# Kernel tuning notes

Hardware: AMD Instinct MI355X
Metric: run time of the kernel (lower is better)

Reference implementation:

```python
import jax, jax.numpy as jnp
import numpy as np
from jax import lax

relu = jax.nn.relu

def _conv2d(x, w, b, stride=1, pad=1):
    y = lax.conv_general_dilated(x, w, (stride, stride), [(pad, pad), (pad, pad)],
                                 dimension_numbers=('NCHW', 'OIHW', 'NCHW'))
    return y + b[None, :, None, None]

def _convT2d(x, wt, b):
    # PyTorch ConvTranspose2d(k=4, stride=2, padding=1) == dilated conv with flipped, transposed weight
    w = jnp.flip(wt, (2, 3)).transpose(1, 0, 2, 3)  # (out,in,4,4)
    y = lax.conv_general_dilated(x, w, (1, 1), [(2, 2), (2, 2)], lhs_dilation=(2, 2),
                                 dimension_numbers=('NCHW', 'OIHW', 'NCHW'))
    return y + b[None, :, None, None]

def _conv3d(x, w, b):
    y = lax.conv_general_dilated(x, w, (1, 1, 1), [(1, 1), (1, 1), (1, 1)],
                                 dimension_numbers=('NCDHW', 'OIDHW', 'NCDHW'))
    return y + b[None, :, None, None, None]

def _bilinear(x, py, px):
    # x: (B,C,H,W); py/px: (B,C,K,H,W) fractional sample coords; zero padding outside
    B, C, H, W = x.shape
    y0 = jnp.floor(py)
    x0 = jnp.floor(px)
    y0i = y0.astype(jnp.int32)
    x0i = x0.astype(jnp.int32)
    wy1 = py - y0
    wx1 = px - x0
    wy0 = 1.0 - wy1
    wx0 = 1.0 - wx1

    def corner(yi, xi):
        valid = (yi >= 0) & (yi < H) & (xi >= 0) & (xi < W)
        yc = jnp.clip(yi, 0, H - 1)
        xc = jnp.clip(xi, 0, W - 1)
        gather = lambda img, yy, xx: img[yy, xx]  # (H,W),(K,H,W)->(K,H,W)
        v = jax.vmap(jax.vmap(gather))(x, yc, xc)
        return jnp.where(valid, v, 0.0)

    return (wy0 * wx0 * corner(y0i, x0i) + wy0 * wx1 * corner(y0i, x0i + 1)
            + wy1 * wx0 * corner(y0i + 1, x0i) + wy1 * wx1 * corner(y0i + 1, x0i + 1))

def _deform_conv(x, off, msk, w, b, ks=3):
    # Modulated deformable conv v2, stride 1, pad ks//2, deformable_groups = C (1 channel/group)
    B, C, H, W = x.shape
    K = ks * ks
    pad = ks // 2
    off = off.reshape(B, C, K, 2, H, W)  # per group/kernel-point (dy, dx)
    dy = off[:, :, :, 0]
    dx = off[:, :, :, 1]
    ki, kj = jnp.meshgrid(jnp.arange(ks), jnp.arange(ks), indexing='ij')
    ky = (ki.reshape(-1) - pad).astype(x.dtype)  # (K,)
    kx = (kj.reshape(-1) - pad).astype(x.dtype)
    gy = jnp.arange(H, dtype=x.dtype)
    gx = jnp.arange(W, dtype=x.dtype)
    py = gy[None, None, None, :, None] + ky[None, None, :, None, None] + dy
    px = gx[None, None, None, None, :] + kx[None, None, :, None, None] + dx
    sampled = _bilinear(x, py, px) * msk.reshape(B, C, K, H, W)  # (B,C,K,H,W)
    out = jnp.einsum('bckhw,ock->bohw', sampled, w.reshape(w.shape[0], C, K))
    return out + b[None, :, None, None]

def _forward(inputs, w_in, b_in, w_dn1a, b_dn1a, w_dn1b, b_dn1b, w_dn2a, b_dn2a, w_dn2b, b_dn2b,
             w_up1a, b_up1a, wt_up1, bt_up1, w_up2a, b_up2a, wt_up2, bt_up2,
             w_tra, b_tra, w_trb, b_trb, wt_tr, bt_tr, w_out, b_out,
             w_tf3a, b_tf3a, w_tf3b, b_tf3b, w_tf2, b_tf2, w_om, b_om, w_dc, b_dc):
    C = inputs.shape[1]
    K = 9
    # U-shape encoder
    f0 = relu(_conv2d(inputs, w_in, b_in))
    f1 = relu(_conv2d(relu(_conv2d(f0, w_dn1a, b_dn1a, stride=2)), w_dn1b, b_dn1b))
    f2 = relu(_conv2d(relu(_conv2d(f1, w_dn2a, b_dn2a, stride=2)), w_dn2b, b_dn2b))
    # trunk
    t = relu(_conv2d(f2, w_tra, b_tra, stride=2))
    t = relu(_conv2d(t, w_trb, b_trb))
    t = relu(_convT2d(t, wt_tr, bt_tr))
    # decoder with skip concats
    t = relu(_conv2d(jnp.concatenate([t, f2], axis=1), w_up2a, b_up2a))
    t = relu(_convT2d(t, wt_up2, bt_up2))
    t = relu(_conv2d(jnp.concatenate([t, f1], axis=1), w_up1a, b_up1a))
    t = relu(_convT2d(t, wt_up1, bt_up1))
    # temporal fusion (Conv3d over frames, mean-pool depth)
    x3 = inputs[:, None]  # (B,1,D,H,W)
    x3 = relu(_conv3d(x3, w_tf3a, b_tf3a))
    x3 = relu(_conv3d(x3, w_tf3b, b_tf3b))
    tf = _conv2d(x3.mean(axis=2), w_tf2, b_tf2)
    fused = relu(t + tf)
    om = _conv2d(relu(_conv2d(fused, w_out, b_out)), w_om, b_om)
    off = om[:, :C * 2 * K]
    msk = jax.nn.sigmoid(om[:, C * 2 * K:])
    return relu(_deform_conv(inputs, off, msk, w_dc, b_dc, 3))

def setup_inputs() -> dict:
    key = jax.random.key(0)
    cnt = [0]
    def rn(shape, scale=0.05):
        cnt[0] += 1
        return scale * jax.random.normal(jax.random.fold_in(key, cnt[0]), shape, dtype=jnp.float32)
    B, C, H, W, nf, out_nc = 2, 7, 160, 160, 32, 64
    z = lambda n: jnp.zeros((n,), jnp.float32)
    d = {'inputs': rn((B, C, H, W), 1.0)}
    d['w_in'] = rn((nf, C, 3, 3)); d['b_in'] = z(nf)
    for i in (1, 2):
        d[f'w_dn{i}a'] = rn((nf, nf, 3, 3)); d[f'b_dn{i}a'] = z(nf)
        d[f'w_dn{i}b'] = rn((nf, nf, 3, 3)); d[f'b_dn{i}b'] = z(nf)
        d[f'w_up{i}a'] = rn((nf, 2 * nf, 3, 3)); d[f'b_up{i}a'] = z(nf)
        d[f'wt_up{i}'] = rn((nf, nf, 4, 4)); d[f'bt_up{i}'] = z(nf)
    d['w_tra'] = rn((nf, nf, 3, 3)); d['b_tra'] = z(nf)
    d['w_trb'] = rn((nf, nf, 3, 3)); d['b_trb'] = z(nf)
    d['wt_tr'] = rn((nf, nf, 4, 4)); d['bt_tr'] = z(nf)
    d['w_out'] = rn((nf, nf, 3, 3)); d['b_out'] = z(nf)
    d['w_tf3a'] = rn((nf, 1, 3, 3, 3)); d['b_tf3a'] = z(nf)
    d['w_tf3b'] = rn((nf, nf, 3, 3, 3)); d['b_tf3b'] = z(nf)
    d['w_tf2'] = rn((nf, nf, 3, 3)); d['b_tf2'] = z(nf)
    d['w_om'] = rn((C * 3 * 9, nf, 3, 3)); d['b_om'] = z(C * 3 * 9)
    d['w_dc'] = rn((out_nc, C, 3, 3)); d['b_dc'] = z(out_nc)
    return d

def reference(inputs, w_in, b_in, w_dn1a, b_dn1a, w_dn1b, b_dn1b, w_dn2a, b_dn2a, w_dn2b, b_dn2b,
              w_up1a, b_up1a, wt_up1, bt_up1, w_up2a, b_up2a, wt_up2, bt_up2,
              w_tra, b_tra, w_trb, b_trb, wt_tr, bt_tr, w_out, b_out,
              w_tf3a, b_tf3a, w_tf3b, b_tf3b, w_tf2, b_tf2, w_om, b_om, w_dc, b_dc):
    return _forward(inputs, w_in, b_in, w_dn1a, b_dn1a, w_dn1b, b_dn1b, w_dn2a, b_dn2a, w_dn2b, b_dn2b,
                    w_up1a, b_up1a, wt_up1, bt_up1, w_up2a, b_up2a, wt_up2, bt_up2,
                    w_tra, b_tra, w_trb, b_trb, wt_tr, bt_tr, w_out, b_out,
                    w_tf3a, b_tf3a, w_tf3b, b_tf3b, w_tf2, b_tf2, w_om, b_om, w_dc, b_dc)
```

## Files before the change

### kernel.cpp

```cpp
#include <hip/hip_runtime.h>
#include <math.h>


#define TPB 256

static inline int nblk(long long total) { return (int)((total + TPB - 1) / TPB); }

typedef short bf16x8 __attribute__((ext_vector_type(8)));
typedef float f32x4 __attribute__((ext_vector_type(4)));

__device__ __forceinline__ unsigned short f2bf(float f) {
    unsigned int u = __float_as_uint(f);
    unsigned int r = u + 0x7FFFu + ((u >> 16) & 1u);
    return (unsigned short)(r >> 16);
}

template <int TB, int RELU, int HAS_RES>
__global__ __launch_bounds__(TB) void conv2d_t4_k(
    const float* __restrict__ in, const float* __restrict__ w,
    const float* __restrict__ bias, const float* __restrict__ res,
    float* __restrict__ out, int B, int Ci, int H, int W, int Co, int BPC) {
    __shared__ float ws_w[32 * 9];
    int co = (blockIdx.x / BPC) % Co;
    int b  = blockIdx.x / (BPC * Co);
// ... 3 lines not shown
    int nq = W >> 2;
    int r = (blockIdx.x % BPC) * TB + threadIdx.x;
    if (r >= H * nq) return;
    int q = r % nq, ho = r / nq;
    int wb = q * 4;
    float bv = bias[co];
    float a0 = bv, a1 = bv, a2 = bv, a3 = bv;
    const float* ipb = in + (size_t)b * Ci * H * W;
    for (int ci = 0; ci < Ci; ++ci) {
        const float* ip = ipb + (size_t)ci * H * W;
        const float* wc = ws_w + ci * 9;
#pragma unroll
        for (int kh = 0; kh < 3; ++kh) {
            int y = ho - 1 + kh;
            if (y < 0 || y >= H) continue;
            const float* row = ip + (size_t)y * W + wb;
            float4 xv = *(const float4*)row;
            float xm = (wb > 0) ? row[-1] : 0.f;
            float xp = (wb + 4 < W) ? row[4] : 0.f;
            float w0 = wc[kh * 3], w1 = wc[kh * 3 + 1], w2 = wc[kh * 3 + 2];
            a0 += xm   * w0 + xv.x * w1 + xv.y * w2;
            a1 += xv.x * w0 + xv.y * w1 + xv.z * w2;
            a2 += xv.y * w0 + xv.z * w1 + xv.w * w2;
            a3 += xv.z * w0 + xv.w * w1 + xp   * w2;
        }
    }
    size_t o = ((size_t)(b * Co + co) * H + ho) * W + wb;
    if (HAS_RES) {
        float4 rv = *(const float4*)(res + o);
        a0 += rv.x; a1 += rv.y; a2 += rv.z; a3 += rv.w;
    }
    if (RELU) { a0 = fmaxf(a0, 0.f); a1 = fmaxf(a1, 0.f); a2 = fmaxf(a2, 0.f); a3 = fmaxf(a3, 0.f); }
    *(float4*)(out + o) = make_float4(a0, a1, a2, a3);
}

template <int RELU, int HAS_RES, int HAS_IN2>
__global__ __launch_bounds__(TPB) void conv2d_c4_k(
    const float* __restrict__ in, const float* __restrict__ in2,
    const float* __restrict__ w, const float* __restrict__ bias,
    const float* __restrict__ res, float* __restrict__ out,
    int B, int Ci, int H, int W, int Co, int COG, int BPC) {
    __shared__ float ws_w[4 * 32 * 9];
    int cog = (blockIdx.x / BPC) % COG;
    int b   = blockIdx.x / (BPC * COG);
    int co0 = cog * 4;
    int nw = Ci * 9;
    for (int i = threadIdx.x; i < 4 * nw; i += TPB) {
        int cr = i / nw; int co = co0 + cr;
        ws_w[i] = (co < Co) ? w[(size_t)co * nw + (i - cr * nw)] : 0.f;
    }
    __syncthreads();
    int nq = W >> 2;
    int r = (blockIdx.x % BPC) * TPB + threadIdx.x;
    if (r >= H * nq) return;
    int q = r % nq, ho = r / nq;
    int wb = q * 4;
    float a[4][4];
#pragma unroll
    for (int cr = 0; cr < 4; ++cr) {
        float bv = (co0 + cr < Co) ? bias[co0 + cr] : 0.f;
        a[cr][0] = bv; a[cr][1] = bv; a[cr][2] = bv; a[cr][3] = bv;
    }
    const float* ipb = in + (size_t)b * Ci * H * W;
    const float* ipb2 = HAS_IN2 ? in2 + (size_t)b * Ci * H * W : nullptr;
    for (int ci = 0; ci < Ci; ++ci) {
        const float* ip = ipb + (size_t)ci * H * W;
        const float* ip2 = HAS_IN2 ? ipb2 + (size_t)ci * H * W : nullptr;
#pragma unroll
        for (int kh = 0; kh < 3; ++kh) {
            int y = ho - 1 + kh;
            if (y < 0 || y >= H) continue;
            const float* row = ip + (size_t)y * W + wb;
            float4 xv = *(const float4*)row;
            float x_[6];
            x_[0] = (wb > 0) ? row[-1] : 0.f;
            x_[5] = (wb + 4 < W) ? row[4] : 0.f;
            if (HAS_IN2) {
                const float* row2 = ip2 + (size_t)y * W + wb;
                float4 x2 = *(const float4*)row2;
                xv.x += x2.x; xv.y += x2.y; xv.z += x2.z; xv.w += x2.w;
                if (wb > 0) x_[0] += row2[-1];
                if (wb + 4 < W) x_[5] += row2[4];
            }
            x_[1] = xv.x; x_[2] = xv.y; x_[3] = xv.z; x_[4] = xv.w;
#pragma unroll
            for (int cr = 0; cr < 4; ++cr) {
                const float* wc = ws_w + cr * nw + ci * 9 + kh * 3;
                float w0 = wc[0], w1 = wc[1], w2 = wc[2];
                a[cr][0] += x_[0] * w0 + x_[1] * w1 + x_[2] * w2;
                a[cr][1] += x_[1] * w0 + x_[2] * w1 + x_[3] * w2;
                a[cr][2] += x_[2] * w0 + x_[3] * w1 + x_[4] * w2;
                a[cr][3] += x_[3] * w0 + x_[4] * w1 + x_[5] * w2;
            }
        }
    }
#pragma unroll
    for (int cr = 0; cr < 4; ++cr) {
        int co = co0 + cr;
        if (co >= Co) break;
        size_t o = ((size_t)(b * Co + co) * H + ho) * W + wb;
        float a0 = a[cr][0], a1 = a[cr][1], a2 = a[cr][2], a3 = a[cr][3];
        if (HAS_RES) {
            float4 rv = *(const float4*)(res + o);
            a0 += rv.x; a1 += rv.y; a2 += rv.z; a3 += rv.w;
        }
        if (RELU) { a0 = fmaxf(a0, 0.f); a1 = fmaxf(a1, 0.f); a2 = fmaxf(a2, 0.f); a3 = fmaxf(a3, 0.f); }
        *(float4*)(out + o) = make_float4(a0, a1, a2, a3);
    }
}

template <int TB>
__global__ __launch_bounds__(TB) void conv2d_s2_t4_k(
    const float* __restrict__ in, const float* __restrict__ w,
    const float* __restrict__ bias, float* __restrict__ out,
    int B, int Ci, int Hi, int Wi, int Co, int BPC) {
    __shared__ float ws_w[32 * 9];
    int Ho = Hi >> 1, Wo = Wi >> 1;
    int co = (blockIdx.x / BPC) % Co;
    int b  = blockIdx.x / (BPC * Co);
    for (int i = threadIdx.x; i < Ci * 9; i += TB)
        ws_w[i] = w[(size_t)co * Ci * 9 + i];
    __syncthreads();
    int nq = Wo >> 2;
    int r = (blockIdx.x % BPC) * TB + threadIdx.x;
    if (r >= Ho * nq) return;
    int q = r % nq, ho = r / nq;
    int wb = q * 4;
    float bv = bias[co];
    float a0 = bv, a1 = bv, a2 = bv, a3 = bv;
    const float* ipb = in + (size_t)b * Ci * Hi * Wi;
    for (int ci = 0; ci < Ci; ++ci) {
        const float* ip = ipb + (size_t)ci * Hi * Wi;
        const float* wc = ws_w + ci * 9;
#pragma unroll
        for (int kh = 0; kh < 3; ++kh) {
            int y = 2 * ho - 1 + kh;
            if (y < 0 || y >= Hi) continue;
            const float* row = ip + (size_t)y * Wi;
            float z0 = (2 * wb - 1 >= 0) ? row[2 * wb - 1] : 0.f;
            float4 za = *(const float4*)(row + 2 * wb);
            float4 zb = *(const float4*)(row + 2 * wb + 4);
// ... 32 lines not shown
    int iy1 = iy0 + 1;
    int ix0 = wb / 2 - 1;
    bool vy0 = (iy0 >= 0) && (iy0 < Hi);
    bool vy1 = (iy1 >= 0) && (iy1 < Hi);
    float bv = bias[co];
    float a0 = bv, a1 = bv, a2 = bv, a3 = bv;
    const float* ipb = in + (size_t)b * C * Hi * Wi;
    for (int ci = 0; ci < C; ++ci) {
        const float* ip = ipb + (size_t)ci * Hi * Wi;
        float u0 = 0, u1 = 0, u2 = 0, u3 = 0, v0 = 0, v1 = 0, v2 = 0, v3 = 0;
        if (vy0) {
            const float* rw = ip + (size_t)iy0 * Wi;
            if (ix0 >= 0) u0 = rw[ix0];
            u1 = rw[ix0 + 1]; u2 = rw[ix0 + 2];
            if (ix0 + 3 < Wi) u3 = rw[ix0 + 3];
        }
        if (vy1) {
            const float* rw = ip + (size_t)iy1 * Wi;
            if (ix0 >= 0) v0 = rw[ix0];
            v1 = rw[ix0 + 1]; v2 = rw[ix0 + 2];
            if (ix0 + 3 < Wi) v3 = rw[ix0 + 3];
        }
        const float* wr0 = ws_w + ci * 16 + (3 - p) * 4;
        const float* wr1 = ws_w + ci * 16 + (1 - p) * 4;
        a0 += u0 * wr0[3] + u1 * wr0[1] + v0 * wr1[3] + v1 * wr1[1];
        a1 += u1 * wr0[2] + u2 * wr0[0] + v1 * wr1[2] + v2 * wr1[0];
        a2 += u1 * wr0[3] + u2 * wr0[1] + v1 * wr1[3] + v2 * wr1[1];
        a3 += u2 * wr0[2] + u3 * wr0[0] + v2 * wr1[2] + v3 * wr1[0];
    }
    size_t o = ((size_t)(b * C + co) * Ho + ho) * Wo + wb;
    *(float4*)(out + o) = make_float4(fmaxf(a0, 0.f), fmaxf(a1, 0.f), fmaxf(a2, 0.f), fmaxf(a3, 0.f));
}

__global__ __launch_bounds__(TPB) void convt2d_c4_k(
    const float* __restrict__ in, const float* __restrict__ wt,
    const float* __restrict__ bias, float* __restrict__ out,
    int B, int C, int Hi, int Wi, int BPC) {
    __shared__ float ws_w[4][32 * 16];
    int Ho = 2 * Hi, Wo = 2 * Wi;
    int cog = (blockIdx.x / BPC) % (C / 4);
    int b   = blockIdx.x / (BPC * (C / 4));
    int co0 = cog * 4;
    for (int i = threadIdx.x; i < 4 * C * 16; i += TPB) {
        int cr = i / (C * 16); int j = i % (C * 16);
        int ci = j >> 4, t = j & 15;
        ws_w[cr][j] = wt[((size_t)ci * C + (co0 + cr)) * 16 + t];
    }
    __syncthreads();
    int nq = Wo >> 2;
    int r = (blockIdx.x % BPC) * TPB + threadIdx.x;
    if (r >= Ho * nq) return;
    int q = r % nq, ho = r / nq;
    int wb = q * 4;
    int p = ho & 1;
    int iy0 = (ho + p) / 2 - 1;
    int iy1 = iy0 + 1;
    int ix0 = wb / 2 - 1;
    bool vy0 = (iy0 >= 0) && (iy0 < Hi);
    bool vy1 = (iy1 >= 0) && (iy1 < Hi);
    float a[4][4];
#pragma unroll
    for (int cr = 0; cr < 4; ++cr) {
        float bv = bias[co0 + cr];
        a[cr][0] = bv; a[cr][1] = bv; a[cr][2] = bv; a[cr][3] = bv;
    }
    const float* ipb = in + (size_t)b * C * Hi * Wi;
    for (int ci = 0; ci < C; ++ci) {
        const float* ip = ipb + (size_t)ci * Hi * Wi;
        float u0 = 0, u1 = 0, u2 = 0, u3 = 0, v0 = 0, v1 = 0, v2 = 0, v3 = 0;
        if (vy0) {
            const float* rw = ip + (size_t)iy0 * Wi;
            if (ix0 >= 0) u0 = rw[ix0];
            u1 = rw[ix0 + 1]; u2 = rw[ix0 + 2];
            if (ix0 + 3 < Wi) u3 = rw[ix0 + 3];
        }
        if (vy1) {
            const float* rw = ip + (size_t)iy1 * Wi;
            if (ix0 >= 0) v0 = rw[ix0];
            v1 = rw[ix0 + 1]; v2 = rw[ix0 + 2];
            if (ix0 + 3 < Wi) v3 = rw[ix0 + 3];
        }
#pragma unroll
        for (int cr = 0; cr < 4; ++cr) {
            const float* wr0 = ws_w[cr] + ci * 16 + (3 - p) * 4;
            const float* wr1 = ws_w[cr] + ci * 16 + (1 - p) * 4;
            a[cr][0] += u0 * wr0[3] + u1 * wr0[1] + v0 * wr1[3] + v1 * wr1[1];
            a[cr][1] += u1 * wr0[2] + u2 * wr0[0] + v1 * wr1[2] + v2 * wr1[0];
            a[cr][2] += u1 * wr0[3] + u2 * wr0[1] + v1 * wr1[3] + v2 * wr1[1];
            a[cr][3] += u2 * wr0[2] + u3 * wr0[0] + v2 * wr1[2] + v3 * wr1[0];
        }
    }
#pragma unroll
    for (int cr = 0; cr < 4; ++cr) {
        size_t o = ((size_t)(b * C + co0 + cr) * Ho + ho) * Wo + wb;
        *(float4*)(out + o) = make_float4(fmaxf(a[cr][0], 0.f), fmaxf(a[cr][1], 0.f),
                                          fmaxf(a[cr][2], 0.f), fmaxf(a[cr][3], 0.f));
    }
}

__global__ void prep_k(const float* __restrict__ wb, const float* __restrict__ wdc,
                       const float* __restrict__ wom, const float* __restrict__ wtf2,
                       const float* __restrict__ wout, const float* __restrict__ wup1a,
                       const float* __restrict__ wup2a,
                       unsigned short* __restrict__ wbf, unsigned short* __restrict__ womf,
                       unsigned short* __restrict__ wtf2f, unsigned short* __restrict__ woutf,
                       unsigned short* __restrict__ wup1f, unsigned short* __restrict__ wup2f,
                       float* __restrict__ wt2, unsigned short* __restrict__ xacl,
                       unsigned short* __restrict__ mcl, unsigned short* __restrict__ tcl,
                       unsigned short* __restrict__ ocl) {
    int i = blockIdx.x * TPB + threadIdx.x;
    if (i < 27648) {
        int j = i & 7;
        int l = (i >> 3) & 63;
        int coH = (i >> 9) & 1;
        int tap = i >> 10;
        int ci = ((l >> 4) << 3) + j;
        int co = (coH << 4) + (l & 15);
        wbf[i] = f2bf(wb[(size_t)(co * 32 + ci) * 27 + tap]);
        return;
    }
    int i2 = i - 27648;
    if (i2 < 4032) {
        int o = i2 & 63, ck = i2 >> 6;
        wt2[i2] = wdc[o * 63 + ck];
        return;
    }
    int i3 = i2 - 4032;
    if (i3 < 20 * 644) {
        int pl = i3 / 644, e = i3 % 644;
        int off;
        if (e < 162)      off = e;
        else if (e < 324) off = 161 * 162 + (e - 162);
        else if (e < 484) off = (e - 324 + 1) * 162;
        else              off = (e - 484 + 1) * 162 + 161;
        unsigned short* base;
        int pl2;
        if (pl < 14)      { base = xacl; pl2 = pl; }
        else if (pl < 16) { base = mcl;  pl2 = pl - 14; }
        else if (pl < 18) { base = tcl;  pl2 = pl - 16; }
        else              { base = ocl;  pl2 = pl - 18; }
        uint4* d = (uint4*)(base + ((size_t)pl2 * 26244 + off) * 32);
        uint4 z = make_uint4(0, 0, 0, 0);
        d[0] = z; d[1] = z; d[2] = z; d[3] = z;
// ... 24 lines not shown
    int i6 = i5 - 9216;
    if (i6 < 9216) {
        int j = i6 & 7;
        int l = (i6 >> 3) & 63;
        int q = i6 >> 9;
        int coH = q & 1, tap = q >> 1;
        int ci = ((l >> 4) << 3) + j;
        int co = coH * 16 + (l & 15);
        woutf[i6] = f2bf(wout[((size_t)co * 32 + ci) * 9 + tap]);
        return;
    }
    int i7 = i6 - 9216;
    if (i7 < 18432) {
        int j = i7 & 7;
        int l = (i7 >> 3) & 63;
        int q = i7 >> 9;
        int coH = q & 1, kc = (q >> 1) & 1, tap = q >> 2;
        int ci = kc * 32 + ((l >> 4) << 3) + j;
        int co = coH * 16 + (l & 15);
        wup1f[i7] = f2bf(wup1a[((size_t)co * 64 + ci) * 9 + tap]);
        return;
    }
    int i8 = i7 - 18432;
    if (i8 >= 18432) return;
    int j = i8 & 7;
    int l = (i8 >> 3) & 63;
    int q = i8 >> 9;
    int coH = q & 1, kc = (q >> 1) & 1, tap = q >> 2;
    int ci = kc * 32 + ((l >> 4) << 3) + j;
    int co = coH * 16 + (l & 15);
    wup2f[i8] = f2bf(wup2a[((size_t)co * 64 + ci) * 9 + tap]);
}

__global__ __launch_bounds__(TPB) void conv3da_cl_k(
    const float* __restrict__ x, const float* __restrict__ wa,
    const float* __restrict__ ba, unsigned short* __restrict__ xacl,
    int B, int H, int W) {
    __shared__ float xin[3 * 3 * 162];
    __shared__ float wsa[864];
    int blk = blockIdx.x;
    int y  = blk % 160;
    int d  = (blk / 160) % 7;
    int b  = blk / 1120;
    int tid = threadIdx.x;
    for (int i = tid; i < 3 * 3 * 162; i += TPB) {
        int xx = i % 162; int t = i / 162; int yy = t % 3; int dz = t / 3;
        int gd = d - 1 + dz, gy = y - 1 + yy, gx = xx - 1;
        float v = 0.f;
        if (gd >= 0 && gd < 7 && gy >= 0 && gy < H && gx >= 0 && gx < W)
            v = x[((size_t)(b * 7 + gd)) * H * W + (size_t)gy * W + gx];
        xin[i] = v;
    }
    for (int i = tid; i < 864; i += TPB) wsa[i] = wa[i];
    __syncthreads();
    int co = tid & 31;
    int xi0 = tid >> 5;
    float bv = ba[co];
    const float* wc = wsa + co * 27;
    size_t rowbase = (((size_t)(b * 7 + d) * 162 + (y + 1)) * 162 + 1) * 32 + co;
    for (int k = 0; k < 20; ++k) {
        int gx = k * 8 + xi0;
        float acc = bv;
#pragma unroll
        for (int dz = 0; dz < 3; ++dz)
#pragma unroll
            for (int yy = 0; yy < 3; ++yy)
#pragma unroll
                for (int kw = 0; kw < 3; ++kw)
                    acc += xin[dz * 486 + yy * 162 + gx + kw] * wc[dz * 9 + yy * 3 + kw];
        xacl[rowbase + (size_t)gx * 32] = f2bf(fmaxf(acc, 0.f));
    }
}

template <int HH, int WW, int PH, int PW>
__global__ __launch_bounds__(TPB) void cat2cl_k(
    const float* __restrict__ a, const float* __restrict__ c2,
    unsigned short* __restrict__ dst) {
    int idx = blockIdx.x * TPB + threadIdx.x;
    if (idx >= 2 * PH * PW) return;
    int pos = idx % (PH * PW);
    int b = idx / (PH * PW);
    int y = pos / PW, x = pos % PW;
    uint4* d = (uint4*)(dst + (size_t)idx * 64);
    if (y == 0 || y > HH || x == 0 || x > WW) {
        uint4 z = make_uint4(0, 0, 0, 0);
#pragma unroll
        for (int k = 0; k < 8; ++k) d[k] = z;
        return;
    }
    size_t off = (size_t)(y - 1) * WW + (x - 1);
    const float* sa = a + (size_t)b * 32 * (HH * WW) + off;
    const float* sc = c2 + (size_t)b * 32 * (HH * WW) + off;
    unsigned int pk[32];
#pragma unroll
    for (int j = 0; j < 16; ++j) {
        float v0 = sa[(size_t)(2 * j) * (HH * WW)];
        float v1 = sa[(size_t)(2 * j + 1) * (HH * WW)];
        pk[j] = (unsigned int)f2bf(v0) | ((unsigned int)f2bf(v1) << 16);
    }
#pragma unroll
    for (int j = 0; j < 16; ++j) {
        float v0 = sc[(size_t)(2 * j) * (HH * WW)];
        float v1 = sc[(size_t)(2 * j + 1) * (HH * WW)];
        pk[16 + j] = (unsigned int)f2bf(v0) | ((unsigned int)f2bf(v1) << 16);
    }
#pragma unroll
    for (int k = 0; k < 8; ++k)
        d[k] = make_uint4(pk[4 * k], pk[4 * k + 1], pk[4 * k + 2], pk[4 * k + 3]);
}

__global__ __launch_bounds__(TPB) void conv3db_mfma_k(
    const unsigned short* __restrict__ xacl, const unsigned short* __restrict__ wbf,
    const float* __restrict__ bb, unsigned short* __restrict__ mcl, int B, int H, int W) {
    int blk = blockIdx.x;
    int b = blk / 800;
    int rem = blk % 800;
    int y = rem / 5;
    int xp = rem % 5;
    int tid = threadIdx.x;
    int l = tid & 63;
    int wv = tid >> 6;
    int mt = wv & 1, coH = wv >> 1;
    int x0 = xp * 32 + mt * 16;
    int co = coH * 16 + (l & 15);
    float bv = bb[co];
    f32x4 acc[7];
#pragma unroll
    for (int d = 0; d < 7; ++d) { acc[d][0] = bv; acc[d][1] = bv; acc[d][2] = bv; acc[d][3] = bv; }

    int ubase = (y * 162 + x0 + (l & 15)) * 32 + ((l >> 4) << 3);
    const unsigned short* xb = xacl + (size_t)b * 5878656;
    const unsigned short* wbase = wbf + ((size_t)coH * 64 + l) * 8;

    for (int j2 = 0; j2 < 9; ++j2) {
        int off2 = (j2 / 3) * 5184 + (j2 % 3) * 32;
        bf16x8 bf0 = *reinterpret_cast<const bf16x8*>(wbase + (size_t)(0 * 9 + j2) * 1024);
        bf16x8 bf1 = *reinterpret_cast<const bf16x8*>(wbase + (size_t)(1 * 9 + j2) * 1024);
        bf16x8 bf2 = *reinterpret_cast<const bf16x8*>(wbase + (size_t)(2 * 9 + j2) * 1024);
#pragma unroll
        for (int dz = 0; dz < 7; ++dz) {
            bf16x8 af = *reinterpret_cast<const bf16x8*>(xb + (size_t)dz * 839808 + ubase + off2);
            if (dz + 1 < 7) acc[dz + 1] = __builtin_amdgcn_mfma_f32_16x16x32_bf16(af, bf0, acc[dz + 1], 0, 0, 0);
            acc[dz] = __builtin_amdgcn_mfma_f32_16x16x32_bf16(af, bf1, acc[dz], 0, 0, 0);
            if (dz - 1 >= 0) acc[dz - 1] = __builtin_amdgcn_mfma_f32_16x16x32_bf16(af, bf2, acc[dz - 1], 0, 0, 0);
        }
    }

    int xo = x0 + ((l >> 4) << 2);
    size_t clbase = ((size_t)b * 26244 + (size_t)(y + 1) * 162 + (xo + 1)) * 32 + co;
#pragma unroll
    for (int r = 0; r < 4; ++r) {
        float s = 0.f;
#pragma unroll
        for (int d = 0; d < 7; ++d) s += fmaxf(acc[d][r], 0.f);
        mcl[clbase + (size_t)r * 32] = f2bf(s * (1.f / 7.f));
    }
}

template <int HAS_RES, int RELU>
__global__ __launch_bounds__(TPB) void conv_nf_mfma_k(
    const unsigned short* __restrict__ icl, const unsigned short* __restrict__ wf,
    const float* __restrict__ bias, const float* __restrict__ res,
    unsigned short* __restrict__ outcl, int B) {
    int blk = blockIdx.x;
    int b = blk / 800;
    int rem = blk % 800;
    int y = rem / 5;
    int xp = rem % 5;
    int tid = threadIdx.x;
    int l = tid & 63;
    int wv = tid >> 6;
    int mt = wv & 1, coH = wv >> 1;
    int x0 = xp * 32 + mt * 16;
    int co = coH * 16 + (l & 15);
    float bv = bias[co];
    f32x4 acc;
    acc[0] = bv; acc[1] = bv; acc[2] = bv; acc[3] = bv;
    int ubase = (y * 162 + x0 + (l & 15)) * 32 + ((l >> 4) << 3);
    const unsigned short* ib = icl + (size_t)b * 839808;
    const unsigned short* wl = wf + (size_t)l * 8;
#pragma unroll
    for (int tap = 0; tap < 9; ++tap) {
        int off = ((tap / 3) * 162 + (tap % 3)) * 32;
        bf16x8 af = *reinterpret_cast<const bf16x8*>(ib + ubase + off);
        bf16x8 bf = *reinterpret_cast<const bf16x8*>(wl + (size_t)(tap * 2 + coH) * 512);
        acc = __builtin_amdgcn_mfma_f32_16x16x32_bf16(af, bf, acc, 0, 0, 0);
    }
    int xo = x0 + ((l >> 4) << 2);
    size_t obase = ((size_t)(b * 32 + co)) * 25600 + (size_t)y * 160 + xo;
// ... 231 lines not shown
    const size_t n40  = (size_t)B * nf * 40 * 40;
    const size_t n20  = (size_t)B * nf * 20 * 20;

    float* ws = (float*)d_ws;
    float* F0    = ws;
    float* TMP80 = F0 + n160;
    float* F1    = TMP80 + n80;
    float* TMP40 = F1 + n80;
    float* F2    = TMP40 + n40;
    float* T20A  = F2 + n40;
    float* T20B  = T20A + n20;
    float* T40   = T20B + n20;
    float* T40B  = T40 + n40;
    float* T80   = T40B + n40;
    float* T80B  = T80 + n80;
    float* T160  = T80B + n80;
    float* TF    = T160 + n160;
    float* XAREG = TF + n160;
    float* OM    = XAREG;
    float* WT2   = XAREG + 11757312;
    unsigned short* WBF    = (unsigned short*)(WT2 + 4032);
    unsigned short* XACL   = WBF + 27648;
    unsigned short* WOMF   = XACL + 11757312;
    unsigned short* OCL    = WOMF + 55296;
    unsigned short* MCL    = OCL + 1679616;
    unsigned short* TCL    = MCL + 1679616;
    unsigned short* CATCL  = TCL + 1679616;
    unsigned short* CATCL2 = CATCL + 860672;
    unsigned short* WTF2F  = CATCL2 + 279552;
    unsigned short* WOUTF  = WTF2F + 9216;
    unsigned short* WUP1F  = WOUTF + 9216;
    unsigned short* WUP2F  = WUP1F + 18432;

    const int bpc160 = 25;
    const int bpc80_128 = 13;
    const int bpc40_64  = 7;
    const int bpc20_64  = 2;

    prep_k<<<nblk(27648 + 4032 + 20 * 644 + 55296 + 9216 + 9216 + 18432 + 18432), TPB, 0, stream>>>(
        w_tf3b, w_dc, w_om, w_tf2, w_out, w_up1a, w_up2a,
        WBF, WOMF, WTF2F, WOUTF, WUP1F, WUP2F, WT2, XACL, MCL, TCL, OCL);
    conv3da_cl_k<<<B * 7 * 160, TPB, 0, stream>>>(inputs, w_tf3a, b_tf3a, XACL, B, H, W);

    conv2d_c4_k<1, 0, 0><<<B * 8 * bpc160, TPB, 0, stream>>>(inputs, nullptr, w_in, b_in, nullptr, F0, B, 7, 160, 160, nf, 8, bpc160);
    conv2d_s2_t4_k<128><<<B * nf * bpc80_128, 128, 0, stream>>>(F0, w_dn1a, b_dn1a, TMP80, B, nf, 160, 160, nf, bpc80_128);
    conv2d_t4_k<128, 1, 0><<<B * nf * bpc80_128, 128, 0, stream>>>(TMP80, w_dn1b, b_dn1b, nullptr, F1, B, nf, 80, 80, nf, bpc80_128);
    conv2d_s2_t4_k<64><<<B * nf * bpc40_64, 64, 0, stream>>>(F1, w_dn2a, b_dn2a, TMP40, B, nf, 80, 80, nf, bpc40_64);
    conv2d_t4_k<64, 1, 0><<<B * nf * bpc40_64, 64, 0, stream>>>(TMP40, w_dn2b, b_dn2b, nullptr, F2, B, nf, 40, 40, nf, bpc40_64);
    conv2d_s2_t4_k<64><<<B * nf * bpc20_64, 64, 0, stream>>>(F2, w_tra, b_tra, T20A, B, nf, 40, 40, nf, bpc20_64);
    conv2d_t4_k<64, 1, 0><<<B * nf * bpc20_64, 64, 0, stream>>>(T20A, w_trb, b_trb, nullptr, T20B, B, nf, 20, 20, nf, bpc20_64);
    convt2d_t4_k<64><<<B * nf * bpc40_64, 64, 0, stream>>>(T20B, wt_tr, bt_tr, T40, B, nf, 20, 20, bpc40_64);
    cat2cl_k<40, 40, 42, 52><<<nblk(2 * 42 * 52), TPB, 0, stream>>>(T40, F2, CATCL2);
    conv_up2a_mfma_k<<<B * 60, TPB, 0, stream>>>(CATCL2, WUP2F, b_up2a, T40B, B);
    convt2d_t4_k<128><<<B * nf * bpc80_128, 128, 0, stream>>>(T40B, wt_up2, bt_up2, T80, B, nf, 40, 40, bpc80_128);
    cat2cl_k<80, 80, 82, 82><<<nblk(2 * 82 * 82), TPB, 0, stream>>>(T80, F1, CATCL);
    conv_up1a_mfma_k<<<B * 200, TPB, 0, stream>>>(CATCL, WUP1F, b_up1a, T80B, B);
    convt2d_c4_k<<<B * 8 * bpc160, TPB, 0, stream>>>(T80B, wt_up1, bt_up1, T160, B, nf, 80, 80, bpc160);

    conv3db_mfma_k<<<B * 800, TPB, 0, stream>>>(XACL, WBF, b_tf3b, MCL, B, H, W);
    conv_nf_mfma_k<1, 1><<<B * 800, TPB, 0, stream>>>(MCL, WTF2F, b_tf2, T160, TCL, B);
    conv_nf_mfma_k<0, 1><<<B * 800, TPB, 0, stream>>>(TCL, WOUTF, b_out, nullptr, OCL, B);
    conv_om_mfma_k<<<B * 1600, TPB, 0, stream>>>(OCL, WOMF, b_om, OM, B);

    deform_conv2_k<<<B * (H * W / 64), TPB, 0, stream>>>(inputs, OM, WT2, b_dc, out, B, H, W);
}
```

Measured before the change: 419.6 us.

## Fuse independent head and mid-stage kernels into combined launches

Weight prep, the first 3D conv and the input conv now run as one launch, with each block choosing its branch from its index. The tf3b 3D conv and the final transposed conv are merged the same way. The goal is to cut launch overhead and tail idling between small independent kernels so they can share the GPU. The cost is that prep and conv3da no longer have a guaranteed order when touching the XACL buffer. Shared memory is also sized for the largest branch, which may lower occupancy for the lighter ones.

```diff
diff --git a/kernel.cpp b/kernel.cpp
--- a/kernel.cpp
+++ b/kernel.cpp
@@ -59,81 +59,6 @@
     }
     if (RELU) { a0 = fmaxf(a0, 0.f); a1 = fmaxf(a1, 0.f); a2 = fmaxf(a2, 0.f); a3 = fmaxf(a3, 0.f); }
     *(float4*)(out + o) = make_float4(a0, a1, a2, a3);
-}
-
-template <int RELU, int HAS_RES, int HAS_IN2>
-__global__ __launch_bounds__(TPB) void conv2d_c4_k(
-    const float* __restrict__ in, const float* __restrict__ in2,
-    const float* __restrict__ w, const float* __restrict__ bias,
-    const float* __restrict__ res, float* __restrict__ out,
-    int B, int Ci, int H, int W, int Co, int COG, int BPC) {
-    __shared__ float ws_w[4 * 32 * 9];
-    int cog = (blockIdx.x / BPC) % COG;
-    int b   = blockIdx.x / (BPC * COG);
-    int co0 = cog * 4;
-    int nw = Ci * 9;
-    for (int i = threadIdx.x; i < 4 * nw; i += TPB) {
-        int cr = i / nw; int co = co0 + cr;
-        ws_w[i] = (co < Co) ? w[(size_t)co * nw + (i - cr * nw)] : 0.f;
-    }
-    __syncthreads();
-    int nq = W >> 2;
-    int r = (blockIdx.x % BPC) * TPB + threadIdx.x;
-    if (r >= H * nq) return;
-    int q = r % nq, ho = r / nq;
-    int wb = q * 4;
-    float a[4][4];
-#pragma unroll
-    for (int cr = 0; cr < 4; ++cr) {
-        float bv = (co0 + cr < Co) ? bias[co0 + cr] : 0.f;
-        a[cr][0] = bv; a[cr][1] = bv; a[cr][2] = bv; a[cr][3] = bv;
-    }
-    const float* ipb = in + (size_t)b * Ci * H * W;
-    const float* ipb2 = HAS_IN2 ? in2 + (size_t)b * Ci * H * W : nullptr;
-    for (int ci = 0; ci < Ci; ++ci) {
-        const float* ip = ipb + (size_t)ci * H * W;
-        const float* ip2 = HAS_IN2 ? ipb2 + (size_t)ci * H * W : nullptr;
-#pragma unroll
-        for (int kh = 0; kh < 3; ++kh) {
-            int y = ho - 1 + kh;
-            if (y < 0 || y >= H) continue;
-            const float* row = ip + (size_t)y * W + wb;
-            float4 xv = *(const float4*)row;
-            float x_[6];
-            x_[0] = (wb > 0) ? row[-1] : 0.f;
-            x_[5] = (wb + 4 < W) ? row[4] : 0.f;
-            if (HAS_IN2) {
-                const float* row2 = ip2 + (size_t)y * W + wb;
-                float4 x2 = *(const float4*)row2;
-                xv.x += x2.x; xv.y += x2.y; xv.z += x2.z; xv.w += x2.w;
-                if (wb > 0) x_[0] += row2[-1];
-                if (wb + 4 < W) x_[5] += row2[4];
-            }
-            x_[1] = xv.x; x_[2] = xv.y; x_[3] = xv.z; x_[4] = xv.w;
-#pragma unroll
-            for (int cr = 0; cr < 4; ++cr) {
-                const float* wc = ws_w + cr * nw + ci * 9 + kh * 3;
-                float w0 = wc[0], w1 = wc[1], w2 = wc[2];
-                a[cr][0] += x_[0] * w0 + x_[1] * w1 + x_[2] * w2;
-                a[cr][1] += x_[1] * w0 + x_[2] * w1 + x_[3] * w2;
-                a[cr][2] += x_[2] * w0 + x_[3] * w1 + x_[4] * w2;
-                a[cr][3] += x_[3] * w0 + x_[4] * w1 + x_[5] * w2;
-            }
-        }
-    }
-#pragma unroll
-    for (int cr = 0; cr < 4; ++cr) {
-        int co = co0 + cr;
-        if (co >= Co) break;
-        size_t o = ((size_t)(b * Co + co) * H + ho) * W + wb;
-        float a0 = a[cr][0], a1 = a[cr][1], a2 = a[cr][2], a3 = a[cr][3];
-        if (HAS_RES) {
-            float4 rv = *(const float4*)(res + o);
-            a0 += rv.x; a1 += rv.y; a2 += rv.z; a3 += rv.w;
-        }
-        if (RELU) { a0 = fmaxf(a0, 0.f); a1 = fmaxf(a1, 0.f); a2 = fmaxf(a2, 0.f); a3 = fmaxf(a3, 0.f); }
-        *(float4*)(out + o) = make_float4(a0, a1, a2, a3);
-    }
 }
 
 template <int TB>
@@ -232,83 +157,18 @@
     *(float4*)(out + o) = make_float4(fmaxf(a0, 0.f), fmaxf(a1, 0.f), fmaxf(a2, 0.f), fmaxf(a3, 0.f));
 }
 
-__global__ __launch_bounds__(TPB) void convt2d_c4_k(
-    const float* __restrict__ in, const float* __restrict__ wt,
-    const float* __restrict__ bias, float* __restrict__ out,
-    int B, int C, int Hi, int Wi, int BPC) {
-    __shared__ float ws_w[4][32 * 16];
-    int Ho = 2 * Hi, Wo = 2 * Wi;
-    int cog = (blockIdx.x / BPC) % (C / 4);
-    int b   = blockIdx.x / (BPC * (C / 4));
-    int co0 = cog * 4;
-    for (int i = threadIdx.x; i < 4 * C * 16; i += TPB) {
-        int cr = i / (C * 16); int j = i % (C * 16);
-        int ci = j >> 4, t = j & 15;
-        ws_w[cr][j] = wt[((size_t)ci * C + (co0 + cr)) * 16 + t];
-    }
-    __syncthreads();
-    int nq = Wo >> 2;
-    int r = (blockIdx.x % BPC) * TPB + threadIdx.x;
-    if (r >= Ho * nq) return;
-    int q = r % nq, ho = r / nq;
-    int wb = q * 4;
-    int p = ho & 1;
-    int iy0 = (ho + p) / 2 - 1;
-    int iy1 = iy0 + 1;
-    int ix0 = wb / 2 - 1;
-    bool vy0 = (iy0 >= 0) && (iy0 < Hi);
-    bool vy1 = (iy1 >= 0) && (iy1 < Hi);
-    float a[4][4];
-#pragma unroll
-    for (int cr = 0; cr < 4; ++cr) {
-        float bv = bias[co0 + cr];
-        a[cr][0] = bv; a[cr][1] = bv; a[cr][2] = bv; a[cr][3] = bv;
-    }
-    const float* ipb = in + (size_t)b * C * Hi * Wi;
-    for (int ci = 0; ci < C; ++ci) {
-        const float* ip = ipb + (size_t)ci * Hi * Wi;
-        float u0 = 0, u1 = 0, u2 = 0, u3 = 0, v0 = 0, v1 = 0, v2 = 0, v3 = 0;
-        if (vy0) {
-            const float* rw = ip + (size_t)iy0 * Wi;
-            if (ix0 >= 0) u0 = rw[ix0];
-            u1 = rw[ix0 + 1]; u2 = rw[ix0 + 2];
-            if (ix0 + 3 < Wi) u3 = rw[ix0 + 3];
-        }
-        if (vy1) {
-            const float* rw = ip + (size_t)iy1 * Wi;
-            if (ix0 >= 0) v0 = rw[ix0];
-            v1 = rw[ix0 + 1]; v2 = rw[ix0 + 2];
-            if (ix0 + 3 < Wi) v3 = rw[ix0 + 3];
-        }
-#pragma unroll
-        for (int cr = 0; cr < 4; ++cr) {
-            const float* wr0 = ws_w[cr] + ci * 16 + (3 - p) * 4;
-            const float* wr1 = ws_w[cr] + ci * 16 + (1 - p) * 4;
-            a[cr][0] += u0 * wr0[3] + u1 * wr0[1] + v0 * wr1[3] + v1 * wr1[1];
-            a[cr][1] += u1 * wr0[2] + u2 * wr0[0] + v1 * wr1[2] + v2 * wr1[0];
-            a[cr][2] += u1 * wr0[3] + u2 * wr0[1] + v1 * wr1[3] + v2 * wr1[1];
-            a[cr][3] += u2 * wr0[2] + u3 * wr0[0] + v2 * wr1[2] + v3 * wr1[0];
-        }
-    }
-#pragma unroll
-    for (int cr = 0; cr < 4; ++cr) {
-        size_t o = ((size_t)(b * C + co0 + cr) * Ho + ho) * Wo + wb;
-        *(float4*)(out + o) = make_float4(fmaxf(a[cr][0], 0.f), fmaxf(a[cr][1], 0.f),
-                                          fmaxf(a[cr][2], 0.f), fmaxf(a[cr][3], 0.f));
-    }
-}
-
-__global__ void prep_k(const float* __restrict__ wb, const float* __restrict__ wdc,
-                       const float* __restrict__ wom, const float* __restrict__ wtf2,
-                       const float* __restrict__ wout, const float* __restrict__ wup1a,
-                       const float* __restrict__ wup2a,
-                       unsigned short* __restrict__ wbf, unsigned short* __restrict__ womf,
-                       unsigned short* __restrict__ wtf2f, unsigned short* __restrict__ woutf,
-                       unsigned short* __restrict__ wup1f, unsigned short* __restrict__ wup2f,
-                       float* __restrict__ wt2, unsigned short* __restrict__ xacl,
-                       unsigned short* __restrict__ mcl, unsigned short* __restrict__ tcl,
-                       unsigned short* __restrict__ ocl) {
-    int i = blockIdx.x * TPB + threadIdx.x;
+
+__device__ __forceinline__ void prep_body(
+    int i, const float* __restrict__ wb, const float* __restrict__ wdc,
+    const float* __restrict__ wom, const float* __restrict__ wtf2,
+    const float* __restrict__ wout, const float* __restrict__ wup1a,
+    const float* __restrict__ wup2a,
+    unsigned short* __restrict__ wbf, unsigned short* __restrict__ womf,
+    unsigned short* __restrict__ wtf2f, unsigned short* __restrict__ woutf,
+    unsigned short* __restrict__ wup1f, unsigned short* __restrict__ wup2f,
+    float* __restrict__ wt2, unsigned short* __restrict__ xacl,
+    unsigned short* __restrict__ mcl, unsigned short* __restrict__ tcl,
+    unsigned short* __restrict__ ocl) {
     if (i < 27648) {
         int j = i & 7;
         int l = (i >> 3) & 63;
@@ -399,17 +259,14 @@
     wup2f[i8] = f2bf(wup2a[((size_t)co * 64 + ci) * 9 + tap]);
 }
 
-__global__ __launch_bounds__(TPB) void conv3da_cl_k(
+__device__ __forceinline__ void conv3da_body(
+    int blk, int tid, float* __restrict__ xin , float* __restrict__ wsa ,
     const float* __restrict__ x, const float* __restrict__ wa,
     const float* __restrict__ ba, unsigned short* __restrict__ xacl,
     int B, int H, int W) {
-    __shared__ float xin[3 * 3 * 162];
-    __shared__ float wsa[864];
-    int blk = blockIdx.x;
     int y  = blk % 160;
     int d  = (blk / 160) % 7;
     int b  = blk / 1120;
-    int tid = threadIdx.x;
     for (int i = tid; i < 3 * 3 * 162; i += TPB) {
         int xx = i % 162; int t = i / 162; int yy = t % 3; int dz = t / 3;
         int gd = d - 1 + dz, gy = y - 1 + yy, gx = xx - 1;
@@ -437,6 +294,223 @@
                     acc += xin[dz * 486 + yy * 162 + gx + kw] * wc[dz * 9 + yy * 3 + kw];
         xacl[rowbase + (size_t)gx * 32] = f2bf(fmaxf(acc, 0.f));
     }
+}
+
+__device__ __forceinline__ void win_body(
+    int blk, int tid, float* __restrict__ ws_w ,
+    const float* __restrict__ in, const float* __restrict__ w,
+    const float* __restrict__ bias, float* __restrict__ out) {
+    const int Ci = 7, H = 160, W = 160, Co = 32, COG = 8, BPC = 25;
+    int cog = (blk / BPC) % COG;
+    int b   = blk / (BPC * COG);
+    int co0 = cog * 4;
+    int nw = Ci * 9;
+    for (int i = tid; i < 4 * nw; i += TPB) {
+        int cr = i / nw; int co = co0 + cr;
+        ws_w[i] = (co < Co) ? w[(size_t)co * nw + (i - cr * nw)] : 0.f;
+    }
+    __syncthreads();
+    int nq = W >> 2;
+    int r = (blk % BPC) * TPB + tid;
+    if (r >= H * nq) return;
+    int q = r % nq, ho = r / nq;
+    int wb = q * 4;
+    float a[4][4];
+#pragma unroll
+    for (int cr = 0; cr < 4; ++cr) {
+        float bv = (co0 + cr < Co) ? bias[co0 + cr] : 0.f;
+        a[cr][0] = bv; a[cr][1] = bv; a[cr][2] = bv; a[cr][3] = bv;
+    }
+    const float* ipb = in + (size_t)b * Ci * H * W;
+    for (int ci = 0; ci < Ci; ++ci) {
+        const float* ip = ipb + (size_t)ci * H * W;
+#pragma unroll
+        for (int kh = 0; kh < 3; ++kh) {
+            int y = ho - 1 + kh;
+            if (y < 0 || y >= H) continue;
+            const float* row = ip + (size_t)y * W + wb;
+            float4 xv = *(const float4*)row;
+            float x_[6];
+            x_[0] = (wb > 0) ? row[-1] : 0.f;
+            x_[5] = (wb + 4 < W) ? row[4] : 0.f;
+            x_[1] = xv.x; x_[2] = xv.y; x_[3] = xv.z; x_[4] = xv.w;
+#pragma unroll
+            for (int cr = 0; cr < 4; ++cr) {
+                const float* wc = ws_w + cr * nw + ci * 9 + kh * 3;
+                float w0 = wc[0], w1 = wc[1], w2 = wc[2];
+                a[cr][0] += x_[0] * w0 + x_[1] * w1 + x_[2] * w2;
+                a[cr][1] += x_[1] * w0 + x_[2] * w1 + x_[3] * w2;
+                a[cr][2] += x_[2] * w0 + x_[3] * w1 + x_[4] * w2;
+                a[cr][3] += x_[3] * w0 + x_[4] * w1 + x_[5] * w2;
+            }
+        }
+    }
+#pragma unroll
+    for (int cr = 0; cr < 4; ++cr) {
+        size_t o = ((size_t)(b * Co + co0 + cr) * H + ho) * W + wb;
+        *(float4*)(out + o) = make_float4(fmaxf(a[cr][0], 0.f), fmaxf(a[cr][1], 0.f),
+                                          fmaxf(a[cr][2], 0.f), fmaxf(a[cr][3], 0.f));
+    }
+}
+
+__global__ __launch_bounds__(TPB) void head_k(
+    const float* __restrict__ x, const float* __restrict__ wa, const float* __restrict__ ba,
+    unsigned short* __restrict__ xacl,
+    const float* __restrict__ w_in, const float* __restrict__ b_in, float* __restrict__ F0,
+    const float* __restrict__ wb, const float* __restrict__ wdc,
+    const float* __restrict__ wom, const float* __restrict__ wtf2,
+    const float* __restrict__ wout, const float* __restrict__ wup1a,
+    const float* __restrict__ wup2a,
+    unsigned short* __restrict__ wbf, unsigned short* __restrict__ womf,
+    unsigned short* __restrict__ wtf2f, unsigned short* __restrict__ woutf,
+    unsigned short* __restrict__ wup1f, unsigned short* __restrict__ wup2f,
+    float* __restrict__ wt2,
+    unsigned short* __restrict__ mcl, unsigned short* __restrict__ tcl,
+    unsigned short* __restrict__ ocl, int B, int H, int W) {
+    __shared__ float smem[2322];
+    int blk = blockIdx.x;
+    int tid = threadIdx.x;
+    if (blk < 2240) {
+        conv3da_body(blk, tid, smem, smem + 1458, x, wa, ba, xacl, B, H, W);
+        return;
+    }
+    blk -= 2240;
+    if (blk < 400) {
+        win_body(blk, tid, smem, x, w_in, b_in, F0);
+        return;
+    }
+    blk -= 400;
+    prep_body(blk * TPB + tid, wb, wdc, wom, wtf2, wout, wup1a, wup2a,
+              wbf, womf, wtf2f, woutf, wup1f, wup2f, wt2, xacl, mcl, tcl, ocl);
+}
+
+__device__ __forceinline__ void conv3db_body(
+    int blk, int tid, const unsigned short* __restrict__ xacl,
+    const unsigned short* __restrict__ wbf, const float* __restrict__ bb,
+    unsigned short* __restrict__ mcl) {
+    int b = blk / 800;
+    int rem = blk % 800;
+    int y = rem / 5;
+    int xp = rem % 5;
+    int l = tid & 63;
+    int wv = tid >> 6;
+    int mt = wv & 1, coH = wv >> 1;
+    int x0 = xp * 32 + mt * 16;
+    int co = coH * 16 + (l & 15);
+    float bv = bb[co];
+    f32x4 acc[7];
+#pragma unroll
+    for (int d = 0; d < 7; ++d) { acc[d][0] = bv; acc[d][1] = bv; acc[d][2] = bv; acc[d][3] = bv; }
+
+    int ubase = (y * 162 + x0 + (l & 15)) * 32 + ((l >> 4) << 3);
+    const unsigned short* xb = xacl + (size_t)b * 5878656;
+    const unsigned short* wbase = wbf + ((size_t)coH * 64 + l) * 8;
+
+    for (int j2 = 0; j2 < 9; ++j2) {
+        int off2 = (j2 / 3) * 5184 + (j2 % 3) * 32;
+        bf16x8 bf0 = *reinterpret_cast<const bf16x8*>(wbase + (size_t)(0 * 9 + j2) * 1024);
+        bf16x8 bf1 = *reinterpret_cast<const bf16x8*>(wbase + (size_t)(1 * 9 + j2) * 1024);
+        bf16x8 bf2 = *reinterpret_cast<const bf16x8*>(wbase + (size_t)(2 * 9 + j2) * 1024);
+#pragma unroll
+        for (int dz = 0; dz < 7; ++dz) {
+            bf16x8 af = *reinterpret_cast<const bf16x8*>(xb + (size_t)dz * 839808 + ubase + off2);
+            if (dz + 1 < 7) acc[dz + 1] = __builtin_amdgcn_mfma_f32_16x16x32_bf16(af, bf0, acc[dz + 1], 0, 0, 0);
+            acc[dz] = __builtin_amdgcn_mfma_f32_16x16x32_bf16(af, bf1, acc[dz], 0, 0, 0);
+            if (dz - 1 >= 0) acc[dz - 1] = __builtin_amdgcn_mfma_f32_16x16x32_bf16(af, bf2, acc[dz - 1], 0, 0, 0);
+        }
+    }
+
+    int xo = x0 + ((l >> 4) << 2);
+    size_t clbase = ((size_t)b * 26244 + (size_t)(y + 1) * 162 + (xo + 1)) * 32 + co;
+#pragma unroll
+    for (int r = 0; r < 4; ++r) {
+        float s = 0.f;
+#pragma unroll
+        for (int d = 0; d < 7; ++d) s += fmaxf(acc[d][r], 0.f);
+        mcl[clbase + (size_t)r * 32] = f2bf(s * (1.f / 7.f));
+    }
+}
+
+__device__ __forceinline__ void convtc4_body(
+    int blk, int tid, float* __restrict__ ws ,
+    const float* __restrict__ in, const float* __restrict__ wt,
+    const float* __restrict__ bias, float* __restrict__ out) {
+    const int C = 32, Hi = 80, Wi = 80, BPC = 25;
+    int Ho = 2 * Hi, Wo = 2 * Wi;
+    int cog = (blk / BPC) % (C / 4);
+    int b   = blk / (BPC * (C / 4));
+    int co0 = cog * 4;
+    for (int i = tid; i < 4 * C * 16; i += TPB) {
+        int cr = i / (C * 16); int j = i % (C * 16);
+        int ci = j >> 4, t = j & 15;
+        ws[cr * 512 + j] = wt[((size_t)ci * C + (co0 + cr)) * 16 + t];
+    }
+    __syncthreads();
+    int nq = Wo >> 2;
+    int r = (blk % BPC) * TPB + tid;
+    if (r >= Ho * nq) return;
+    int q = r % nq, ho = r / nq;
+    int wb = q * 4;
+    int p = ho & 1;
+    int iy0 = (ho + p) / 2 - 1;
+    int iy1 = iy0 + 1;
+    int ix0 = wb / 2 - 1;
+    bool vy0 = (iy0 >= 0) && (iy0 < Hi);
+    bool vy1 = (iy1 >= 0) && (iy1 < Hi);
+    float a[4][4];
+#pragma unroll
+    for (int cr = 0; cr < 4; ++cr) {
+        float bv = bias[co0 + cr];
+        a[cr][0] = bv; a[cr][1] = bv; a[cr][2] = bv; a[cr][3] = bv;
+    }
+    const float* ipb = in + (size_t)b * C * Hi * Wi;
+    for (int ci = 0; ci < C; ++ci) {
+        const float* ip = ipb + (size_t)ci * Hi * Wi;
+        float u0 = 0, u1 = 0, u2 = 0, u3 = 0, v0 = 0, v1 = 0, v2 = 0, v3 = 0;
+        if (vy0) {
+            const float* rw = ip + (size_t)iy0 * Wi;
+            if (ix0 >= 0) u0 = rw[ix0];
+            u1 = rw[ix0 + 1]; u2 = rw[ix0 + 2];
+            if (ix0 + 3 < Wi) u3 = rw[ix0 + 3];
+        }
+        if (vy1) {
+            const float* rw = ip + (size_t)iy1 * Wi;
+            if (ix0 >= 0) v0 = rw[ix0];
+            v1 = rw[ix0 + 1]; v2 = rw[ix0 + 2];
+            if (ix0 + 3 < Wi) v3 = rw[ix0 + 3];
+        }
+#pragma unroll
+        for (int cr = 0; cr < 4; ++cr) {
+            const float* wr0 = ws + cr * 512 + ci * 16 + (3 - p) * 4;
+            const float* wr1 = ws + cr * 512 + ci * 16 + (1 - p) * 4;
+            a[cr][0] += u0 * wr0[3] + u1 * wr0[1] + v0 * wr1[3] + v1 * wr1[1];
+            a[cr][1] += u1 * wr0[2] + u2 * wr0[0] + v1 * wr1[2] + v2 * wr1[0];
+            a[cr][2] += u1 * wr0[3] + u2 * wr0[1] + v1 * wr1[3] + v2 * wr1[1];
+            a[cr][3] += u2 * wr0[2] + u3 * wr0[0] + v2 * wr1[2] + v3 * wr1[0];
+        }
+    }
+#pragma unroll
+    for (int cr = 0; cr < 4; ++cr) {
+        size_t o = ((size_t)(b * C + co0 + cr) * Ho + ho) * Wo + wb;
+        *(float4*)(out + o) = make_float4(fmaxf(a[cr][0], 0.f), fmaxf(a[cr][1], 0.f),
+                                          fmaxf(a[cr][2], 0.f), fmaxf(a[cr][3], 0.f));
+    }
+}
+
+__global__ __launch_bounds__(TPB) void mid_k(
+    const unsigned short* __restrict__ xacl, const unsigned short* __restrict__ wbf,
+    const float* __restrict__ bb, unsigned short* __restrict__ mcl,
+    const float* __restrict__ t80b, const float* __restrict__ wt_up1,
+    const float* __restrict__ bt_up1, float* __restrict__ t160, int B) {
+    __shared__ float smem[2048];
+    int blk = blockIdx.x;
+    int tid = threadIdx.x;
+    if (blk < B * 800) {
+        conv3db_body(blk, tid, xacl, wbf, bb, mcl);
+        return;
+    }
+    blk -= B * 800;
+    convtc4_body(blk, tid, smem, t80b, wt_up1, bt_up1, t160);
 }
 
 template <int HH, int WW, int PH, int PW>
@@ -474,54 +548,6 @@
 #pragma unroll
     for (int k = 0; k < 8; ++k)
         d[k] = make_uint4(pk[4 * k], pk[4 * k + 1], pk[4 * k + 2], pk[4 * k + 3]);
-}
-
-__global__ __launch_bounds__(TPB) void conv3db_mfma_k(
-    const unsigned short* __restrict__ xacl, const unsigned short* __restrict__ wbf,
-    const float* __restrict__ bb, unsigned short* __restrict__ mcl, int B, int H, int W) {
-    int blk = blockIdx.x;
-    int b = blk / 800;
-    int rem = blk % 800;
-    int y = rem / 5;
-    int xp = rem % 5;
-    int tid = threadIdx.x;
-    int l = tid & 63;
-    int wv = tid >> 6;
-    int mt = wv & 1, coH = wv >> 1;
-    int x0 = xp * 32 + mt * 16;
-    int co = coH * 16 + (l & 15);
-    float bv = bb[co];
-    f32x4 acc[7];
-#pragma unroll
-    for (int d = 0; d < 7; ++d) { acc[d][0] = bv; acc[d][1] = bv; acc[d][2] = bv; acc[d][3] = bv; }
-
-    int ubase = (y * 162 + x0 + (l & 15)) * 32 + ((l >> 4) << 3);
-    const unsigned short* xb = xacl + (size_t)b * 5878656;
-    const unsigned short* wbase = wbf + ((size_t)coH * 64 + l) * 8;
-
-    for (int j2 = 0; j2 < 9; ++j2) {
-        int off2 = (j2 / 3) * 5184 + (j2 % 3) * 32;
-        bf16x8 bf0 = *reinterpret_cast<const bf16x8*>(wbase + (size_t)(0 * 9 + j2) * 1024);
-        bf16x8 bf1 = *reinterpret_cast<const bf16x8*>(wbase + (size_t)(1 * 9 + j2) * 1024);
-        bf16x8 bf2 = *reinterpret_cast<const bf16x8*>(wbase + (size_t)(2 * 9 + j2) * 1024);
-#pragma unroll
-        for (int dz = 0; dz < 7; ++dz) {
-            bf16x8 af = *reinterpret_cast<const bf16x8*>(xb + (size_t)dz * 839808 + ubase + off2);
-            if (dz + 1 < 7) acc[dz + 1] = __builtin_amdgcn_mfma_f32_16x16x32_bf16(af, bf0, acc[dz + 1], 0, 0, 0);
-            acc[dz] = __builtin_amdgcn_mfma_f32_16x16x32_bf16(af, bf1, acc[dz], 0, 0, 0);
-            if (dz - 1 >= 0) acc[dz - 1] = __builtin_amdgcn_mfma_f32_16x16x32_bf16(af, bf2, acc[dz - 1], 0, 0, 0);
-        }
-    }
-
-    int xo = x0 + ((l >> 4) << 2);
-    size_t clbase = ((size_t)b * 26244 + (size_t)(y + 1) * 162 + (xo + 1)) * 32 + co;
-#pragma unroll
-    for (int r = 0; r < 4; ++r) {
-        float s = 0.f;
-#pragma unroll
-        for (int d = 0; d < 7; ++d) s += fmaxf(acc[d][r], 0.f);
-        mcl[clbase + (size_t)r * 32] = f2bf(s * (1.f / 7.f));
-    }
 }
 
 template <int HAS_RES, int RELU>
@@ -819,17 +845,16 @@
     unsigned short* WUP1F  = WOUTF + 9216;
     unsigned short* WUP2F  = WUP1F + 18432;
 
-    const int bpc160 = 25;
     const int bpc80_128 = 13;
     const int bpc40_64  = 7;
     const int bpc20_64  = 2;
 
-    prep_k<<<nblk(27648 + 4032 + 20 * 644 + 55296 + 9216 + 9216 + 18432 + 18432), TPB, 0, stream>>>(
+    const int PREP_NB = nblk(27648 + 4032 + 20 * 644 + 55296 + 9216 + 9216 + 18432 + 18432);
+    head_k<<<2240 + 400 + PREP_NB, TPB, 0, stream>>>(
+        inputs, w_tf3a, b_tf3a, XACL, w_in, b_in, F0,
         w_tf3b, w_dc, w_om, w_tf2, w_out, w_up1a, w_up2a,
-        WBF, WOMF, WTF2F, WOUTF, WUP1F, WUP2F, WT2, XACL, MCL, TCL, OCL);
-    conv3da_cl_k<<<B * 7 * 160, TPB, 0, stream>>>(inputs, w_tf3a, b_tf3a, XACL, B, H, W);
-
-    conv2d_c4_k<1, 0, 0><<<B * 8 * bpc160, TPB, 0, stream>>>(inputs, nullptr, w_in, b_in, nullptr, F0, B, 7, 160, 160, nf, 8, bpc160);
+        WBF, WOMF, WTF2F, WOUTF, WUP1F, WUP2F, WT2, MCL, TCL, OCL, B, H, W);
+
     conv2d_s2_t4_k<128><<<B * nf * bpc80_128, 128, 0, stream>>>(F0, w_dn1a, b_dn1a, TMP80, B, nf, 160, 160, nf, bpc80_128);
     conv2d_t4_k<128, 1, 0><<<B * nf * bpc80_128, 128, 0, stream>>>(TMP80, w_dn1b, b_dn1b, nullptr, F1, B, nf, 80, 80, nf, bpc80_128);
     conv2d_s2_t4_k<64><<<B * nf * bpc40_64, 64, 0, stream>>>(F1, w_dn2a, b_dn2a, TMP40, B, nf, 80, 80, nf, bpc40_64);
@@ -842,9 +867,9 @@
     convt2d_t4_k<128><<<B * nf * bpc80_128, 128, 0, stream>>>(T40B, wt_up2, bt_up2, T80, B, nf, 40, 40, bpc80_128);
     cat2cl_k<80, 80, 82, 82><<<nblk(2 * 82 * 82), TPB, 0, stream>>>(T80, F1, CATCL);
     conv_up1a_mfma_k<<<B * 200, TPB, 0, stream>>>(CATCL, WUP1F, b_up1a, T80B, B);
-    convt2d_c4_k<<<B * 8 * bpc160, TPB, 0, stream>>>(T80B, wt_up1, bt_up1, T160, B, nf, 80, 80, bpc160);
-
-    conv3db_mfma_k<<<B * 800, TPB, 0, stream>>>(XACL, WBF, b_tf3b, MCL, B, H, W);
+
+    mid_k<<<B * 800 + 400, TPB, 0, stream>>>(XACL, WBF, b_tf3b, MCL, T80B, wt_up1, bt_up1, T160, B);
+
     conv_nf_mfma_k<1, 1><<<B * 800, TPB, 0, stream>>>(MCL, WTF2F, b_tf2, T160, TCL, B);
     conv_nf_mfma_k<0, 1><<<B * 800, TPB, 0, stream>>>(TCL, WOUTF, b_out, nullptr, OCL, B);
     conv_om_mfma_k<<<B * 1600, TPB, 0, stream>>>(OCL, WOMF, b_om, OM, B);
```

Result: faster. 402.2 us (-4.2%).
